# Kernel tuning notes

Measured on AMD Instinct MI355X. Metric: run time of the kernel, lower is better.

## Reference

```python
import jax, jax.numpy as jnp
import numpy as np

D_MODEL = 384
D_INNER = 768          # expand * d_model
NHEADS = 12            # d_inner // headdim
HEADDIM = 64
DSTATE = 64
CONV_DIM = D_INNER + 2 * DSTATE       # 896
D_IN_PROJ = 2 * D_INNER + 2 * DSTATE + NHEADS  # 1676
LN_EPS = 1e-5


def _avg_pool_3x3(x):
    # 3x3 avg pool, stride 1, SAME padding, count_include_pad=False
    sums = jax.lax.reduce_window(x, 0.0, jax.lax.add, (1, 1, 3, 3), (1, 1, 1, 1), 'SAME')
    ones = jnp.ones((1, 1) + x.shape[2:], x.dtype)
    cnt = jax.lax.reduce_window(ones, 0.0, jax.lax.add, (1, 1, 3, 3), (1, 1, 1, 1), 'SAME')
    return sums / cnt


def setup_inputs() -> dict:
    key = jax.random.key(0)
    ks = jax.random.split(key, 8)
    B, H, W = 8, 56, 56
    L = H * W
    # dt_bias init as in the torch module
    dt = jnp.exp(jax.random.uniform(ks[5], (NHEADS,)) * (np.log(0.1) - np.log(0.001)) + np.log(0.001))
    dt = jnp.clip(dt, 1e-4, None)
    dt_bias = dt + jnp.log(-jnp.expm1(-dt))
    A_log = jnp.log(jax.random.uniform(ks[6], (D_INNER,), minval=1.0, maxval=16.0))
    return {
        'x': jax.random.normal(ks[0], (B, L, D_MODEL), jnp.float32),
        'in_proj_w': jax.random.normal(ks[1], (D_IN_PROJ, D_MODEL), jnp.float32) * 0.05,
        'conv_w': jax.random.normal(ks[2], (CONV_DIM, 1, 3, 3), jnp.float32) * 0.1,
        'conv_b': jnp.zeros((CONV_DIM,), jnp.float32),
        'dt_bias': dt_bias,
        'A_log': A_log,
        'D': jnp.ones((NHEADS,), jnp.float32),
        'norm_w': jnp.ones((D_INNER,), jnp.float32),
        'norm_b': jnp.zeros((D_INNER,), jnp.float32),
        'out_proj_w': jax.random.normal(ks[3], (D_MODEL, D_INNER), jnp.float32) * 0.05,
        'H': H,
        'W': W,
    }


def reference(x, in_proj_w, conv_w, conv_b, dt_bias, A_log, D, norm_w, norm_b, out_proj_w, H, W):
    B, L, _ = x.shape
    # in_proj and split: z | xBC | dt
    zxbcdt = x @ in_proj_w.T                                   # (B, L, 1676)
    z = zxbcdt[..., :D_INNER]                                   # (B, L, 768)
    xBC = zxbcdt[..., D_INNER:D_INNER + CONV_DIM]               # (B, L, 896)
    dt = jax.nn.softplus(zxbcdt[..., D_INNER + CONV_DIM:] + dt_bias)  # (B, L, 12)
    # depthwise 3x3 conv over the HxW grid + SiLU
    xBC_img = xBC.reshape(B, H, W, CONV_DIM).transpose(0, 3, 1, 2)
    xBC_img = jax.lax.conv_general_dilated(
        xBC_img, conv_w, (1, 1), 'SAME', feature_group_count=CONV_DIM)
    xBC_img = xBC_img + conv_b[None, :, None, None]
    xBC = jax.nn.silu(xBC_img).transpose(0, 2, 3, 1).reshape(B, L, CONV_DIM)
    xs = xBC[..., :D_INNER].reshape(B, L, NHEADS, HEADDIM)
    Bm = xBC[..., D_INNER:D_INNER + DSTATE]                     # (B, L, dstate)
    Cm = xBC[..., D_INNER + DSTATE:]                            # (B, L, dstate)
    # ssm_op (ngroups == 1, pattern == 'LoDSA')
    A = -jnp.exp(A_log).reshape(NHEADS, HEADDIM)                # (h, d)
    x_in = xs.transpose(0, 2, 1, 3)                             # (B, h, L, d)
    dA = dt.transpose(0, 2, 1)[..., None] * A[None, :, None, :] # (B, h, L, d)
    dx = dA * x_in                                              # (B, h, L, d)
    # (B,h,L,d) -> (B,h,H,W,d) -> (B, h*d, H, W), pool, back
    dx_img = dx.reshape(B, NHEADS, H, W, HEADDIM).transpose(0, 1, 4, 2, 3)
    dx_img = dx_img.reshape(B, NHEADS * HEADDIM, H, W)
    dx_pool = _avg_pool_3x3(dx_img)
    dx = dx_pool.reshape(B, NHEADS, HEADDIM, L).transpose(0, 1, 3, 2)  # (B, h, L, d)
    # linear-attention style global aggregation (replaces the scan)
    h_state = jnp.einsum('bls,bhld->bhsd', Bm, dx)              # (B, h, s, d)
    Ch = jnp.einsum('bls,bhsd->bhld', Cm, h_state)              # (B, h, L, d)
    y = Ch + x_in * D[None, :, None, None]
    y = y.transpose(0, 2, 1, 3).reshape(B, L, D_INNER)
    # gated layernorm + out projection
    g = y * jax.nn.silu(z)
    mu = g.mean(-1, keepdims=True)
    var = ((g - mu) ** 2).mean(-1, keepdims=True)
    gn = (g - mu) / jnp.sqrt(var + LN_EPS) * norm_w + norm_b
    return gn @ out_proj_w.T
```

## Files before the change

kernel.cpp:

```cpp
#include <hip/hip_runtime.h>
#include <hip/hip_bf16.h>
#include <math.h>

#define BB 8
#define HH 56
#define WW 56
#define LL (HH*WW)
#define DMODEL 384
#define DINNER 768
#define NH 12
#define HD 64
#define DS 64
#define CDIM (DINNER + 2*DS)
#define NPROJ (2*DINNER + 2*DS + NH)
#define NPAD 1792
#define MTOT (BB*LL)
#define LN_EPS 1e-5f
#define NCG (CDIM/8)
#define NDG (DINNER/8)
#define SPLITL 7

typedef __attribute__((ext_vector_type(8))) _Float16 f16x8;
typedef __attribute__((ext_vector_type(4))) float f32x4;

__device__ __forceinline__ ushort f2hu(float v) {
    union { _Float16 h; ushort u; } cv; cv.h = (_Float16)v; return cv.u;
}
__device__ __forceinline__ float hu2f(ushort u) {
    union { ushort u; _Float16 h; } cv; cv.u = u; return (float)cv.h;
}

__global__ __launch_bounds__(256) void k_cast_x(
    const float4* __restrict__ in, ushort4* __restrict__ out)
{
    int i = blockIdx.x * 256 + threadIdx.x;
    float4 v = in[i];
    ushort4 h;
    h.x = f2hu(v.x); h.y = f2hu(v.y); h.z = f2hu(v.z); h.w = f2hu(v.w);
    out[i] = h;
}

#define W1Q (NPAD*DMODEL/4)
#define W2Q (DMODEL*DINNER/4)
__global__ __launch_bounds__(256) void k_cast_w(
    const float* __restrict__ w1src, const float* __restrict__ w2src,
    ushort4* __restrict__ w1dst, ushort4* __restrict__ w2dst)
{
    int i = blockIdx.x * 256 + threadIdx.x;
    if (i < W1Q) {
        int n = i / (DMODEL / 4);
        int k = (i % (DMODEL / 4)) * 4;
        ushort4 h = {0,0,0,0};
        if (n < NPROJ) {
            float4 v = *(const float4*)(w1src + (size_t)n * DMODEL + k);
            h.x = f2hu(v.x); h.y = f2hu(v.y); h.z = f2hu(v.z); h.w = f2hu(v.w);
        }
        w1dst[i] = h;
    } else {
        int t = i - W1Q;
        float4 v = ((const float4*)w2src)[t];
        ushort4 h;
        h.x = f2hu(v.x); h.y = f2hu(v.y); h.z = f2hu(v.z); h.w = f2hu(v.w);
        w2dst[t] = h;
    }
}

#define LDSW 40
__global__ __launch_bounds__(256) void k_gemm1_mfma(
    const ushort* __restrict__ xh, const ushort* __restrict__ wh,
    const float* __restrict__ dt_bias,
    ushort* __restrict__ zbuf, ushort* __restrict__ xbcbuf, float* __restrict__ dtbuf)
{
    __shared__ ushort As[2][128 * LDSW];
    __shared__ ushort Bs[2][128 * LDSW];
    const int m0 = blockIdx.y * 128;
    const int n0 = blockIdx.x * 128;
    const int tid = threadIdx.x;
    const int wid = tid >> 6;
    const int lane = tid & 63;
    const int r = lane & 15;
    const int quad = lane >> 4;
    const int wm = (wid >> 1) * 64;
    const int wn = (wid & 1) * 64;
    const int srow = tid >> 2;
    const int scol = (tid & 3) * 8;

    f32x4 acc[4][4];
#pragma unroll
    for (int i = 0; i < 4; ++i)
#pragma unroll
        for (int j = 0; j < 4; ++j) acc[i][j] = (f32x4){0.f, 0.f, 0.f, 0.f};

    {
        int4 a0 = *(const int4*)(xh + (size_t)(m0 + srow)      * DMODEL + scol);
        int4 a1 = *(const int4*)(xh + (size_t)(m0 + srow + 64) * DMODEL + scol);
        int4 b0 = *(const int4*)(wh + (size_t)(n0 + srow)      * DMODEL + scol);
        int4 b1 = *(const int4*)(wh + (size_t)(n0 + srow + 64) * DMODEL + scol);
        *(int4*)(As[0] + srow * LDSW + scol)        = a0;
        *(int4*)(As[0] + (srow + 64) * LDSW + scol) = a1;
        *(int4*)(Bs[0] + srow * LDSW + scol)        = b0;
        *(int4*)(Bs[0] + (srow + 64) * LDSW + scol) = b1;
    }
    __syncthreads();

    int cur = 0;
    for (int k0 = 32; k0 <= DMODEL; k0 += 32) {
        const bool has = (k0 < DMODEL);
        int4 na0, na1, nb0, nb1;
        if (has) {
            na0 = *(const int4*)(xh + (size_t)(m0 + srow)      * DMODEL + k0 + scol);
            na1 = *(const int4*)(xh + (size_t)(m0 + srow + 64) * DMODEL + k0 + scol);
            nb0 = *(const int4*)(wh + (size_t)(n0 + srow)      * DMODEL + k0 + scol);
            nb1 = *(const int4*)(wh + (size_t)(n0 + srow + 64) * DMODEL + k0 + scol);
        }
        f16x8 af[4], bfr[4];
#pragma unroll
        for (int t = 0; t < 4; ++t) {
            af[t]  = *(const f16x8*)(As[cur] + (wm + t * 16 + r) * LDSW + quad * 8);
            bfr[t] = *(const f16x8*)(Bs[cur] + (wn + t * 16 + r) * LDSW + quad * 8);
        }
#pragma unroll
        for (int i = 0; i < 4; ++i)
#pragma unroll
            for (int j = 0; j < 4; ++j)
                acc[i][j] = __builtin_amdgcn_mfma_f32_16x16x32_f16(af[i], bfr[j], acc[i][j], 0, 0, 0);
        if (has) {
            *(int4*)(As[cur ^ 1] + srow * LDSW + scol)        = na0;
            *(int4*)(As[cur ^ 1] + (srow + 64) * LDSW + scol) = na1;
            *(int4*)(Bs[cur ^ 1] + srow * LDSW + scol)        = nb0;
            *(int4*)(Bs[cur ^ 1] + (srow + 64) * LDSW + scol) = nb1;
            __syncthreads();
            cur ^= 1;
        }
    }
#pragma unroll
    for (int i = 0; i < 4; ++i) {
#pragma unroll
        for (int j = 0; j < 4; ++j) {
            int n = n0 + wn + j * 16 + r;
            if (n >= NPROJ) continue;
#pragma unroll
            for (int v = 0; v < 4; ++v) {
                int m = m0 + wm + i * 16 + quad * 4 + v;
                float val = acc[i][j][v];
                if (n < DINNER) {
                    zbuf[(size_t)m * DINNER + n] = f2hu(val);
                } else if (n < DINNER + CDIM) {
                    xbcbuf[(size_t)m * CDIM + (n - DINNER)] = f2hu(val);
                } else {
                    int h = n - (DINNER + CDIM);
                    float t = val + dt_bias[h];
                    float sp = (t > 20.f) ? t : log1pf(expf(t));
                    dtbuf[(size_t)m * NH + h] = sp;
                }
            }
        }
    }
}

__global__ __launch_bounds__(256) void k_gemm2_mfma(
    const ushort* __restrict__ gn, const ushort* __restrict__ wh,
    float* __restrict__ out)
{
    __shared__ ushort As[2][128 * LDSW];
    __shared__ ushort Bs[2][128 * LDSW];
    const int m0 = blockIdx.y * 128;
    const int n0 = blockIdx.x * 128;
    const int tid = threadIdx.x;
    const int wid = tid >> 6;
    const int lane = tid & 63;
    const int r = lane & 15;
    const int quad = lane >> 4;
    const int wm = (wid >> 1) * 64;
    const int wn = (wid & 1) * 64;
    const int srow = tid >> 2;
    const int scol = (tid & 3) * 8;

    f32x4 acc[4][4];
#pragma unroll
    for (int i = 0; i < 4; ++i)
#pragma unroll
        for (int j = 0; j < 4; ++j) acc[i][j] = (f32x4){0.f, 0.f, 0.f, 0.f};

    {
        int4 a0 = *(const int4*)(gn + (size_t)(m0 + srow)      * DINNER + scol);
        int4 a1 = *(const int4*)(gn + (size_t)(m0 + srow + 64) * DINNER + scol);
        int4 b0 = *(const int4*)(wh + (size_t)(n0 + srow)      * DINNER + scol);
        int4 b1 = *(const int4*)(wh + (size_t)(n0 + srow + 64) * DINNER + scol);
        *(int4*)(As[0] + srow * LDSW + scol)        = a0;
        *(int4*)(As[0] + (srow + 64) * LDSW + scol) = a1;
        *(int4*)(Bs[0] + srow * LDSW + scol)        = b0;
        *(int4*)(Bs[0] + (srow + 64) * LDSW + scol) = b1;
    }
    __syncthreads();

    int cur = 0;
    for (int k0 = 32; k0 <= DINNER; k0 += 32) {
        const bool has = (k0 < DINNER);
        int4 na0, na1, nb0, nb1;
        if (has) {
            na0 = *(const int4*)(gn + (size_t)(m0 + srow)      * DINNER + k0 + scol);
            na1 = *(const int4*)(gn + (size_t)(m0 + srow + 64) * DINNER + k0 + scol);
            nb0 = *(const int4*)(wh + (size_t)(n0 + srow)      * DINNER + k0 + scol);
            nb1 = *(const int4*)(wh + (size_t)(n0 + srow + 64) * DINNER + k0 + scol);
        }
        f16x8 af[4], bfr[4];
#pragma unroll
        for (int t = 0; t < 4; ++t) {
            af[t]  = *(const f16x8*)(As[cur] + (wm + t * 16 + r) * LDSW + quad * 8);
            bfr[t] = *(const f16x8*)(Bs[cur] + (wn + t * 16 + r) * LDSW + quad * 8);
        }
#pragma unroll
        for (int i = 0; i < 4; ++i)
#pragma unroll
            for (int j = 0; j < 4; ++j)
                acc[i][j] = __builtin_amdgcn_mfma_f32_16x16x32_f16(af[i], bfr[j], acc[i][j], 0, 0, 0);
        if (has) {
            *(int4*)(As[cur ^ 1] + srow * LDSW + scol)        = na0;
            *(int4*)(As[cur ^ 1] + (srow + 64) * LDSW + scol) = na1;
            *(int4*)(Bs[cur ^ 1] + srow * LDSW + scol)        = nb0;
            *(int4*)(Bs[cur ^ 1] + (srow + 64) * LDSW + scol) = nb1;
            __syncthreads();
            cur ^= 1;
        }
    }
#pragma unroll
    for (int i = 0; i < 4; ++i) {
#pragma unroll
        for (int j = 0; j < 4; ++j) {
            int n = n0 + wn + j * 16 + r;
#pragma unroll
            for (int v = 0; v < 4; ++v) {
                int m = m0 + wm + i * 16 + quad * 4 + v;
                out[(size_t)m * DMODEL + n] = acc[i][j][v];
            }
        }
    }
}

__global__ __launch_bounds__(256) void k_conv(
    const ushort* __restrict__ xbc, const float* __restrict__ cw,
    const float* __restrict__ cb, ushort* __restrict__ out)
{
    const int gid = blockIdx.x * 256 + threadIdx.x;
    const int cg  = gid % NCG;
    const int pix = gid / NCG;
    const int b = pix / LL, ij = pix % LL;
    const int i = ij / WW, j = ij % WW;
    const int c0 = cg * 8;

    float wreg[72];
#pragma unroll
    for (int t = 0; t < 18; ++t)
        *(float4*)(wreg + t * 4) = *(const float4*)(cw + c0 * 9 + t * 4);
    float acc[8];
    {
        float4 b0 = *(const float4*)(cb + c0);
        float4 b1 = *(const float4*)(cb + c0 + 4);
        acc[0]=b0.x; acc[1]=b0.y; acc[2]=b0.z; acc[3]=b0.w;
        acc[4]=b1.x; acc[5]=b1.y; acc[6]=b1.z; acc[7]=b1.w;
    }
#pragma unroll
    for (int ky = 0; ky < 3; ++ky) {
        int ii = i + ky - 1;
        if (ii < 0 || ii >= HH) continue;
#pragma unroll
        for (int kx = 0; kx < 3; ++kx) {
            int jj = j + kx - 1;
            if (jj < 0 || jj >= WW) continue;
            union { int4 q; ushort u[8]; } xv;
            xv.q = *(const int4*)(xbc + ((size_t)b * LL + ii * WW + jj) * CDIM + c0);
            int t = ky * 3 + kx;
#pragma unroll
            for (int q = 0; q < 8; ++q)
                acc[q] += wreg[q * 9 + t] * hu2f(xv.u[q]);
        }
    }
    union { int4 q; ushort u[8]; } o;
#pragma unroll
    for (int q = 0; q < 8; ++q) {
        float s = acc[q] / (1.f + expf(-acc[q]));
        o.u[q] = f2hu(s);
    }
    *(int4*)(out + (size_t)pix * CDIM + c0) = o.q;
}

__global__ __launch_bounds__(256) void k_dxpool(
    const ushort* __restrict__ xbc_conv, const float* __restrict__ dtbuf,
    const float* __restrict__ A_log, ushort* __restrict__ dxp)
{
    const int gid = blockIdx.x * 256 + threadIdx.x;
    const int cg  = gid % NDG;
    const int pix = gid / NDG;
    const int b = pix / LL, l = pix % LL;
    const int i = l / WW, j = l % WW;
    const int c0 = cg * 8;
    const int h = c0 >> 6;

    float Ah[8];
    {
        float4 a0 = *(const float4*)(A_log + c0);
        float4 a1 = *(const float4*)(A_log + c0 + 4);
        Ah[0]=a0.x; Ah[1]=a0.y; Ah[2]=a0.z; Ah[3]=a0.w;
        Ah[4]=a1.x; Ah[5]=a1.y; Ah[6]=a1.z; Ah[7]=a1.w;
    }
#pragma unroll
    for (int q = 0; q < 8; ++q) Ah[q] = -expf(Ah[q]);

    float sum[8] = {0.f,0.f,0.f,0.f,0.f,0.f,0.f,0.f};
    int cnt = 0;
#pragma unroll
    for (int dy = -1; dy <= 1; ++dy) {
        int ii = i + dy;
        if (ii < 0 || ii >= HH) continue;
#pragma unroll
        for (int dxx = -1; dxx <= 1; ++dxx) {
            int jj = j + dxx;
            if (jj < 0 || jj >= WW) continue;
            int ll = ii * WW + jj;
            ++cnt;
            float dtv = dtbuf[((size_t)b * LL + ll) * NH + h];
            union { int4 q; ushort u[8]; } xv;
            xv.q = *(const int4*)(xbc_conv + ((size_t)b * LL + ll) * CDIM + c0);
#pragma unroll
            for (int q = 0; q < 8; ++q)
                sum[q] += dtv * hu2f(xv.u[q]);
        }
    }
    float inv = 1.f / (float)cnt;
    union { int4 q; ushort u[8]; } o;
#pragma unroll
    for (int q = 0; q < 8; ++q)
        o.u[q] = f2hu(Ah[q] * sum[q] * inv);
    *(int4*)(dxp + (((size_t)b * NH + h) * LL + l) * HD + (c0 & 63)) = o.q;
}

#define LDSP 33
__global__ __launch_bounds__(256) void k_hstate_mfma(
    const ushort* __restrict__ xbc_conv, const ushort* __restrict__ dxp,
    float* __restrict__ hpart)
{
    __shared__ ushort DsT[64 * LDSP];
    __shared__ ushort BsT[64 * LDSP];
    const int lc = blockIdx.x;
    const int bh = blockIdx.y;
    const int b = bh / NH;
    const int tid = threadIdx.x;
    const int wid = tid >> 6;
    const int lane = tid & 63;
    const int r = lane & 15;
    const int quad = lane >> 4;
    const int wd = (wid >> 1) * 32;
    const int wsn = (wid & 1) * 32;
    const int lt = tid >> 3;
    const int sg = (tid & 7) * 8;

    f32x4 acc[2][2];
#pragma unroll
    for (int i = 0; i < 2; ++i)
#pragma unroll
        for (int j = 0; j < 2; ++j) acc[i][j] = (f32x4){0.f, 0.f, 0.f, 0.f};

    const int l_base = lc * (LL / SPLITL);
    for (int step = 0; step < (LL / SPLITL) / 32; ++step) {
        int l0 = l_base + step * 32;
        union { int4 q; ushort u[8]; } dv, bv;
        dv.q = *(const int4*)(dxp + (((size_t)bh) * LL + l0 + lt) * HD + sg);
        bv.q = *(const int4*)(xbc_conv + ((size_t)(b * LL + l0 + lt)) * CDIM + DINNER + sg);
        __syncthreads();
#pragma unroll
        for (int q = 0; q < 8; ++q) {
            DsT[(sg + q) * LDSP + lt] = dv.u[q];
            BsT[(sg + q) * LDSP + lt] = bv.u[q];
        }
        __syncthreads();
        f16x8 af[2], bf[2];
#pragma unroll
        for (int t = 0; t < 2; ++t) {
            af[t] = *(const f16x8*)(DsT + (wd + t * 16 + r) * LDSP + quad * 8);
            bf[t] = *(const f16x8*)(BsT + (wsn + t * 16 + r) * LDSP + quad * 8);
        }
#pragma unroll
        for (int i = 0; i < 2; ++i)
#pragma unroll
            for (int j = 0; j < 2; ++j)
                acc[i][j] = __builtin_amdgcn_mfma_f32_16x16x32_f16(af[i], bf[j], acc[i][j], 0, 0, 0);
    }
    float* outp = hpart + ((size_t)(lc * 96 + bh) << 12);
#pragma unroll
    for (int i = 0; i < 2; ++i)
#pragma unroll
        for (int j = 0; j < 2; ++j)
#pragma unroll
            for (int v = 0; v < 4; ++v)
                outp[(wd + i * 16 + quad * 4 + v) * 64 + (wsn + j * 16 + r)] = acc[i][j][v];
}

__global__ __launch_bounds__(256) void k_hprep(
    const float* __restrict__ hpart, ushort* __restrict__ hT)
{
    int i = blockIdx.x * 256 + threadIdx.x;
    int bh = i >> 12;
    int rem = i & 4095;
    float v = 0.f;
#pragma unroll
    for (int lc = 0; lc < SPLITL; ++lc)
        v += hpart[((size_t)(lc * 96 + bh) << 12) + rem];
    hT[i] = f2hu(v);
}

#define HTW 72
__global__ __launch_bounds__(256) void k_chy_mfma(
    const ushort* __restrict__ xbc_conv, const ushort* __restrict__ hT,
    const float* __restrict__ Dp, ushort* __restrict__ ybuf)
{
    __shared__ ushort Hs[64 * HTW];
    const int bh = blockIdx.y;
    const int b = bh / NH, h = bh % NH;
    const int tid = threadIdx.x;
    const int wid = tid >> 6;
    const int lane = tid & 63;
    const int r = lane & 15;
    const int quad = lane >> 4;

    for (int idx = tid; idx < 512; idx += 256) {
        int row = idx >> 3, c8 = (idx & 7) * 8;
        *(int4*)(Hs + row * HTW + c8) = *(const int4*)(hT + ((size_t)bh << 12) + row * 64 + c8);
    }
    __syncthreads();

    const int chunk = blockIdx.x * 4 + wid;
    if (chunk >= 49) return;
    const int l0 = chunk * 64;

    f32x4 acc[4][4];
#pragma unroll
    for (int i = 0; i < 4; ++i)
#pragma unroll
        for (int j = 0; j < 4; ++j) acc[i][j] = (f32x4){0.f, 0.f, 0.f, 0.f};

#pragma unroll
    for (int kk = 0; kk < 2; ++kk) {
        f16x8 af[4], bfr[4];
#pragma unroll
        for (int t = 0; t < 4; ++t) {
            af[t] = *(const f16x8*)(xbc_conv +
                ((size_t)(b * LL + l0 + t * 16 + r)) * CDIM + DINNER + DS + kk * 32 + quad * 8);
            bfr[t] = *(const f16x8*)(Hs + (t * 16 + r) * HTW + kk * 32 + quad * 8);
        }
#pragma unroll
        for (int i = 0; i < 4; ++i)
#pragma unroll
            for (int j = 0; j < 4; ++j)
                acc[i][j] = __builtin_amdgcn_mfma_f32_16x16x32_f16(af[i], bfr[j], acc[i][j], 0, 0, 0);
    }
    const float Dh = Dp[h];
#pragma unroll
    for (int i = 0; i < 4; ++i) {
#pragma unroll
        for (int j = 0; j < 4; ++j) {
            int d = j * 16 + r;
#pragma unroll
            for (int v = 0; v < 4; ++v) {
                int l = l0 + i * 16 + quad * 4 + v;
                float xv = hu2f(xbc_conv[((size_t)(b * LL + l)) * CDIM + h * HD + d]);
                ybuf[((size_t)(b * LL + l)) * DINNER + h * HD + d] = f2hu(acc[i][j][v] + xv * Dh);
            }
        }
    }
}

__global__ __launch_bounds__(256) void k_gln(
    const ushort* __restrict__ ybuf, const ushort* __restrict__ zbuf,
    const float* __restrict__ nw, const float* __restrict__ nb,
    ushort* __restrict__ gnbuf)
{
    const int row = blockIdx.x * 4 + (threadIdx.x >> 6);
    const int lane = threadIdx.x & 63;
    const size_t base = (size_t)row * DINNER;

    float g[12];
    float sum = 0.f, sumsq = 0.f;
#pragma unroll
    for (int p = 0; p < 3; ++p) {
        int c = lane * 4 + p * 256;
        union { ushort4 q; ushort u[4]; } yv, zv;
        yv.q = *(const ushort4*)(ybuf + base + c);
        zv.q = *(const ushort4*)(zbuf + base + c);
#pragma unroll
        for (int q = 0; q < 4; ++q) {
            float y = hu2f(yv.u[q]);
            float z = hu2f(zv.u[q]);
            float gv = y * (z / (1.f + expf(-z)));
            g[p * 4 + q] = gv;
            sum += gv;
            sumsq += gv * gv;
        }
    }
#pragma unroll
    for (int off = 32; off > 0; off >>= 1) {
        sum += __shfl_xor(sum, off, 64);
        sumsq += __shfl_xor(sumsq, off, 64);
    }
    const float mu = sum / (float)DINNER;
    const float var = sumsq / (float)DINNER - mu * mu;
    const float rstd = rsqrtf(var + LN_EPS);
#pragma unroll
    for (int p = 0; p < 3; ++p) {
        int c = lane * 4 + p * 256;
        float4 w = *(const float4*)(nw + c);
        float4 bb = *(const float4*)(nb + c);
        union { ushort4 q; ushort u[4]; } o;
        o.u[0] = f2hu((g[p*4+0] - mu) * rstd * w.x + bb.x);
        o.u[1] = f2hu((g[p*4+1] - mu) * rstd * w.y + bb.y);
        o.u[2] = f2hu((g[p*4+2] - mu) * rstd * w.z + bb.z);
        o.u[3] = f2hu((g[p*4+3] - mu) * rstd * w.w + bb.w);
        *(ushort4*)(gnbuf + base + c) = o.q;
    }
}

extern "C" void kernel_launch(void* const* d_in, const int* in_sizes, int n_in,
                              void* d_out, int out_size, void* d_ws, size_t ws_size,
                              hipStream_t stream)
{
    const float* x         = (const float*)d_in[0];
    const float* in_proj_w = (const float*)d_in[1];
    const float* conv_w    = (const float*)d_in[2];
    const float* conv_b    = (const float*)d_in[3];
    const float* dt_bias   = (const float*)d_in[4];
    const float* A_log     = (const float*)d_in[5];
    const float* Dp        = (const float*)d_in[6];
    const float* norm_w    = (const float*)d_in[7];
    const float* norm_b    = (const float*)d_in[8];
    const float* out_proj_w= (const float*)d_in[9];

    char* wsb = (char*)d_ws;
    float*  dtbuf   = (float*) (wsb + 0);
    ushort* w1      = (ushort*)(wsb + 2777088);
    ushort* w2      = (ushort*)(wsb + 4153344);
    ushort* zbuf    = (ushort*)(wsb + 4743168);
    ushort* xbcraw  = (ushort*)(wsb + 43278336);
    ushort* xbcconv = (ushort*)(wsb + 88236032);
    ushort* x16     = xbcconv;
    ushort* hT      = xbcraw;
    float*  hpart   = (float*)(wsb + 44851200);
    ushort* dxp     = (ushort*)d_out;
    ushort* ybuf    = (ushort*)d_out;
    ushort* gnbuf   = xbcraw;

    k_cast_x <<<MTOT * DMODEL / 4 / 256, 256, 0, stream>>>(
        (const float4*)x, (ushort4*)x16);
    k_cast_w<<<(W1Q + W2Q) / 256, 256, 0, stream>>>(
        in_proj_w, out_proj_w, (ushort4*)w1, (ushort4*)w2);

    k_gemm1_mfma<<<dim3(NPAD / 128, MTOT / 128), 256, 0, stream>>>(
        x16, w1, dt_bias, zbuf, xbcraw, dtbuf);

    k_conv<<<MTOT * NCG / 256, 256, 0, stream>>>(
        xbcraw, conv_w, conv_b, xbcconv);
    k_dxpool<<<MTOT * NDG / 256, 256, 0, stream>>>(
        xbcconv, dtbuf, A_log, dxp);
    k_hstate_mfma<<<dim3(SPLITL, BB * NH), 256, 0, stream>>>(
        xbcconv, dxp, hpart);
    k_hprep<<<96 * 4096 / 256, 256, 0, stream>>>(hpart, hT);
    k_chy_mfma<<<dim3(13, BB * NH), 256, 0, stream>>>(
        xbcconv, hT, Dp, ybuf);
    k_gln<<<MTOT / 4, 256, 0, stream>>>(
        ybuf, zbuf, norm_w, norm_b, gnbuf);
    k_gemm2_mfma<<<dim3(DMODEL / 128, MTOT / 128), 256, 0, stream>>>(
        gnbuf, w2, (float*)d_out);
}
```

Before: 411.8 us.

## Register-block conv and dxpool over four adjacent pixels with tap-major weights

The depthwise conv and the dt-scaled avg-pool kernels now have each thread compute four horizontally adjacent pixels. Each thread loads a 6-column strip per row once and reuses it across three taps, instead of reloading nine neighbours per pixel. Conv weights are re-laid out tap-major during the weight-cast kernel, so each row's weights come in as contiguous float4 loads. This cuts redundant global/L2 loads and index arithmetic, but raises register pressure and reduces the thread count by four.

New measurement: 365.9 us. 11.1% less time.

```diff
diff --git a/kernel.cpp b/kernel.cpp
--- a/kernel.cpp
+++ b/kernel.cpp
@@ -42,9 +42,12 @@
 
 #define W1Q (NPAD*DMODEL/4)
 #define W2Q (DMODEL*DINNER/4)
+#define CWQ (NCG*72/4)
 __global__ __launch_bounds__(256) void k_cast_w(
     const float* __restrict__ w1src, const float* __restrict__ w2src,
-    ushort4* __restrict__ w1dst, ushort4* __restrict__ w2dst)
+    const float* __restrict__ cwsrc,
+    ushort4* __restrict__ w1dst, ushort4* __restrict__ w2dst,
+    float* __restrict__ cwrdst)
 {
     int i = blockIdx.x * 256 + threadIdx.x;
     if (i < W1Q) {
@@ -56,12 +59,22 @@
             h.x = f2hu(v.x); h.y = f2hu(v.y); h.z = f2hu(v.z); h.w = f2hu(v.w);
         }
         w1dst[i] = h;
-    } else {
+    } else if (i < W1Q + W2Q) {
         int t = i - W1Q;
         float4 v = ((const float4*)w2src)[t];
         ushort4 h;
         h.x = f2hu(v.x); h.y = f2hu(v.y); h.z = f2hu(v.z); h.w = f2hu(v.w);
         w2dst[t] = h;
+    } else if (i < W1Q + W2Q + CWQ) {
+        int t = i - W1Q - W2Q;
+#pragma unroll
+        for (int k = 0; k < 4; ++k) {
+            int e = 4 * t + k;
+            int cgx = e / 72;
+            int rr = e % 72;
+            int tap = rr >> 3, q = rr & 7;
+            cwrdst[e] = cwsrc[(cgx * 8 + q) * 9 + tap];
+        }
     }
 }
 
@@ -239,50 +252,70 @@
 }
 
 __global__ __launch_bounds__(256) void k_conv(
-    const ushort* __restrict__ xbc, const float* __restrict__ cw,
+    const ushort* __restrict__ xbc, const float* __restrict__ cwr,
     const float* __restrict__ cb, ushort* __restrict__ out)
 {
     const int gid = blockIdx.x * 256 + threadIdx.x;
     const int cg  = gid % NCG;
-    const int pix = gid / NCG;
-    const int b = pix / LL, ij = pix % LL;
-    const int i = ij / WW, j = ij % WW;
-    const int c0 = cg * 8;
-
-    float wreg[72];
-#pragma unroll
-    for (int t = 0; t < 18; ++t)
-        *(float4*)(wreg + t * 4) = *(const float4*)(cw + c0 * 9 + t * 4);
-    float acc[8];
+    const int pq  = gid / NCG;
+    const int b   = pq / (LL / 4);
+    const int rem = pq % (LL / 4);
+    const int i   = rem / (WW / 4);
+    const int j0  = (rem % (WW / 4)) * 4;
+    const int c0  = cg * 8;
+
+    float acc[4][8];
     {
         float4 b0 = *(const float4*)(cb + c0);
         float4 b1 = *(const float4*)(cb + c0 + 4);
-        acc[0]=b0.x; acc[1]=b0.y; acc[2]=b0.z; acc[3]=b0.w;
-        acc[4]=b1.x; acc[5]=b1.y; acc[6]=b1.z; acc[7]=b1.w;
-    }
+#pragma unroll
+        for (int p = 0; p < 4; ++p) {
+            acc[p][0]=b0.x; acc[p][1]=b0.y; acc[p][2]=b0.z; acc[p][3]=b0.w;
+            acc[p][4]=b1.x; acc[p][5]=b1.y; acc[p][6]=b1.z; acc[p][7]=b1.w;
+        }
+    }
+    const size_t rowbase = (size_t)b * LL;
 #pragma unroll
     for (int ky = 0; ky < 3; ++ky) {
         int ii = i + ky - 1;
         if (ii < 0 || ii >= HH) continue;
-#pragma unroll
-        for (int kx = 0; kx < 3; ++kx) {
-            int jj = j + kx - 1;
-            if (jj < 0 || jj >= WW) continue;
-            union { int4 q; ushort u[8]; } xv;
-            xv.q = *(const int4*)(xbc + ((size_t)b * LL + ii * WW + jj) * CDIM + c0);
-            int t = ky * 3 + kx;
-#pragma unroll
-            for (int q = 0; q < 8; ++q)
-                acc[q] += wreg[q * 9 + t] * hu2f(xv.u[q]);
-        }
-    }
-    union { int4 q; ushort u[8]; } o;
-#pragma unroll
-    for (int q = 0; q < 8; ++q) {
-        float s = acc[q] / (1.f + expf(-acc[q]));
-        o.u[q] = f2hu(s);
-    }
-    *(int4*)(out + (size_t)pix * CDIM + c0) = o.q;
+        float w[24];
+        const float* wr = cwr + (cg * 9 + ky * 3) * 8;
+#pragma unroll
+        for (int t = 0; t < 6; ++t)
+            *(float4*)(w + t * 4) = *(const float4*)(wr + t * 4);
+        float xc[6][8];
+#pragma unroll
+        for (int col = 0; col < 6; ++col) {
+            int jj = j0 - 1 + col;
+            if (jj >= 0 && jj < WW) {
+                union { int4 q; ushort u[8]; } xv;
+                xv.q = *(const int4*)(xbc + (rowbase + ii * WW + jj) * CDIM + c0);
+#pragma unroll
+                for (int q = 0; q < 8; ++q) xc[col][q] = hu2f(xv.u[q]);
+            } else {
+#pragma unroll
+                for (int q = 0; q < 8; ++q) xc[col][q] = 0.f;
+            }
+        }
+#pragma unroll
+        for (int p = 0; p < 4; ++p)
+#pragma unroll
+            for (int kx = 0; kx < 3; ++kx)
+#pragma unroll
+                for (int q = 0; q < 8; ++q)
+                    acc[p][q] += w[kx * 8 + q] * xc[p + kx][q];
+    }
+#pragma unroll
+    for (int p = 0; p < 4; ++p) {
+        union { int4 q; ushort u[8]; } o;
+#pragma unroll
+        for (int q = 0; q < 8; ++q) {
+            float s = acc[p][q] / (1.f + expf(-acc[p][q]));
+            o.u[q] = f2hu(s);
+        }
+        *(int4*)(out + (rowbase + i * WW + j0 + p) * CDIM + c0) = o.q;
+    }
 }
 
 __global__ __launch_bounds__(256) void k_dxpool(
@@ -291,11 +324,13 @@
 {
     const int gid = blockIdx.x * 256 + threadIdx.x;
     const int cg  = gid % NDG;
-    const int pix = gid / NDG;
-    const int b = pix / LL, l = pix % LL;
-    const int i = l / WW, j = l % WW;
-    const int c0 = cg * 8;
-    const int h = c0 >> 6;
+    const int pq  = gid / NDG;
+    const int b   = pq / (LL / 4);
+    const int rem = pq % (LL / 4);
+    const int i   = rem / (WW / 4);
+    const int j0  = (rem % (WW / 4)) * 4;
+    const int c0  = cg * 8;
+    const int h   = c0 >> 6;
 
     float Ah[8];
     {
@@ -307,32 +342,54 @@
 #pragma unroll
     for (int q = 0; q < 8; ++q) Ah[q] = -expf(Ah[q]);
 
-    float sum[8] = {0.f,0.f,0.f,0.f,0.f,0.f,0.f,0.f};
-    int cnt = 0;
-#pragma unroll
-    for (int dy = -1; dy <= 1; ++dy) {
-        int ii = i + dy;
+    float sum[4][8];
+#pragma unroll
+    for (int p = 0; p < 4; ++p)
+#pragma unroll
+        for (int q = 0; q < 8; ++q) sum[p][q] = 0.f;
+
+    const size_t rowbase = (size_t)b * LL;
+#pragma unroll
+    for (int ky = 0; ky < 3; ++ky) {
+        int ii = i + ky - 1;
         if (ii < 0 || ii >= HH) continue;
-#pragma unroll
-        for (int dxx = -1; dxx <= 1; ++dxx) {
-            int jj = j + dxx;
-            if (jj < 0 || jj >= WW) continue;
-            int ll = ii * WW + jj;
-            ++cnt;
-            float dtv = dtbuf[((size_t)b * LL + ll) * NH + h];
-            union { int4 q; ushort u[8]; } xv;
-            xv.q = *(const int4*)(xbc_conv + ((size_t)b * LL + ll) * CDIM + c0);
-#pragma unroll
-            for (int q = 0; q < 8; ++q)
-                sum[q] += dtv * hu2f(xv.u[q]);
-        }
-    }
-    float inv = 1.f / (float)cnt;
-    union { int4 q; ushort u[8]; } o;
-#pragma unroll
-    for (int q = 0; q < 8; ++q)
-        o.u[q] = f2hu(Ah[q] * sum[q] * inv);
-    *(int4*)(dxp + (((size_t)b * NH + h) * LL + l) * HD + (c0 & 63)) = o.q;
+        float dtv[6];
+        float xc[6][8];
+#pragma unroll
+        for (int col = 0; col < 6; ++col) {
+            int jj = j0 - 1 + col;
+            if (jj >= 0 && jj < WW) {
+                dtv[col] = dtbuf[(rowbase + ii * WW + jj) * NH + h];
+                union { int4 q; ushort u[8]; } xv;
+                xv.q = *(const int4*)(xbc_conv + (rowbase + ii * WW + jj) * CDIM + c0);
+#pragma unroll
+                for (int q = 0; q < 8; ++q) xc[col][q] = hu2f(xv.u[q]);
+            } else {
+                dtv[col] = 0.f;
+#pragma unroll
+                for (int q = 0; q < 8; ++q) xc[col][q] = 0.f;
+            }
+        }
+#pragma unroll
+        for (int p = 0; p < 4; ++p)
+#pragma unroll
+            for (int kx = 0; kx < 3; ++kx)
+#pragma unroll
+                for (int q = 0; q < 8; ++q)
+                    sum[p][q] += dtv[p + kx] * xc[p + kx][q];
+    }
+    const int rv = 3 - (i == 0) - (i == HH - 1);
+#pragma unroll
+    for (int p = 0; p < 4; ++p) {
+        int j = j0 + p;
+        int cv = 3 - (j == 0) - (j == WW - 1);
+        float inv = 1.f / (float)(rv * cv);
+        union { int4 q; ushort u[8]; } o;
+#pragma unroll
+        for (int q = 0; q < 8; ++q)
+            o.u[q] = f2hu(Ah[q] * sum[p][q] * inv);
+        *(int4*)(dxp + (((size_t)b * NH + h) * LL + i * WW + j) * HD + (c0 & 63)) = o.q;
+    }
 }
 
 #define LDSP 33
@@ -536,6 +593,7 @@
 
     char* wsb = (char*)d_ws;
     float*  dtbuf   = (float*) (wsb + 0);
+    float*  cwr     = (float*) (wsb + 1204224);
     ushort* w1      = (ushort*)(wsb + 2777088);
     ushort* w2      = (ushort*)(wsb + 4153344);
     ushort* zbuf    = (ushort*)(wsb + 4743168);
@@ -550,15 +608,15 @@
 
     k_cast_x <<<MTOT * DMODEL / 4 / 256, 256, 0, stream>>>(
         (const float4*)x, (ushort4*)x16);
-    k_cast_w<<<(W1Q + W2Q) / 256, 256, 0, stream>>>(
-        in_proj_w, out_proj_w, (ushort4*)w1, (ushort4*)w2);
+    k_cast_w<<<(W1Q + W2Q + CWQ + 255) / 256, 256, 0, stream>>>(
+        in_proj_w, out_proj_w, conv_w, (ushort4*)w1, (ushort4*)w2, cwr);
 
     k_gemm1_mfma<<<dim3(NPAD / 128, MTOT / 128), 256, 0, stream>>>(
         x16, w1, dt_bias, zbuf, xbcraw, dtbuf);
 
-    k_conv<<<MTOT * NCG / 256, 256, 0, stream>>>(
-        xbcraw, conv_w, conv_b, xbcconv);
-    k_dxpool<<<MTOT * NDG / 256, 256, 0, stream>>>(
+    k_conv<<<MTOT / 4 * NCG / 256, 256, 0, stream>>>(
+        xbcraw, cwr, conv_b, xbcconv);
+    k_dxpool<<<MTOT / 4 * NDG / 256, 256, 0, stream>>>(
         xbcconv, dtbuf, A_log, dxp);
     k_hstate_mfma<<<dim3(SPLITL, BB * NH), 256, 0, stream>>>(
         xbcconv, dxp, hpart);
```
